# Optimization experiments

Measured on AMD Instinct MI355X. Metric: run time of the kernel, lower is better.

## Reference

```python
import jax, jax.numpy as jnp
import numpy as np

EMB, HID, SEQ = 768, 512, 2048
BATCH = 2
EPS = 1e-6
LN_EPS = 1e-5
ROPE_BASE = 10000.0
NEG_BIG = -1e9  # stands in for -inf diagonal mask (identical entmax output, NaN-safe)


def rotate_half(x):
    d = x.shape[-1] // 2
    return jnp.concatenate([-x[..., d:], x[..., :d]], axis=-1)


def rope_tables(L, D, dtype=jnp.float32):
    inv_freq = 1.0 / (ROPE_BASE ** (jnp.arange(0, D, 2, dtype=jnp.float32) / D))
    t = jnp.arange(L, dtype=jnp.float32)
    freqs = jnp.outer(t, inv_freq)            # [L, D/2]
    emb = jnp.concatenate([freqs, freqs], -1)  # [L, D]
    return jnp.cos(emb).astype(dtype), jnp.sin(emb).astype(dtype)


def layernorm(x, gamma, beta):
    mu = jnp.mean(x, axis=-1, keepdims=True)
    var = jnp.mean(jnp.square(x - mu), axis=-1, keepdims=True)
    return (x - mu) * jax.lax.rsqrt(var + LN_EPS) * gamma + beta


def entmax15(z):
    """Exact 1.5-entmax along last axis (Peters & Martins sort algorithm)."""
    z = z / 2.0
    z = z - jnp.max(z, axis=-1, keepdims=True)
    zs = -jnp.sort(-z, axis=-1)                      # descending
    L = z.shape[-1]
    k = jnp.arange(1, L + 1, dtype=z.dtype)
    cum = jnp.cumsum(zs, axis=-1)
    cum2 = jnp.cumsum(zs * zs, axis=-1)
    mean = cum / k
    ss = cum2 - cum * mean                           # k*(E[x^2]-E[x]^2)
    delta = (1.0 - ss) / k
    tau = mean - jnp.sqrt(jnp.maximum(delta, 0.0))
    support = jnp.sum((tau <= zs).astype(jnp.int32), axis=-1)
    tau_star = jnp.take_along_axis(tau, (support - 1)[..., None], axis=-1)
    return jnp.square(jnp.maximum(z - tau_star, 0.0))


def setup_inputs() -> dict:
    key = jax.random.key(0)
    ks = jax.random.split(key, 3)
    x = jax.random.normal(ks[0], (BATCH, SEQ, EMB), dtype=jnp.float32)
    Wq = jax.random.normal(ks[1], (HID, EMB), dtype=jnp.float32) / np.sqrt(EMB)
    Wk = jax.random.normal(ks[2], (HID, EMB), dtype=jnp.float32) / np.sqrt(EMB)
    return {
        "x": x, "Wq": Wq, "Wk": Wk,
        "q_gamma": jnp.ones((HID,), jnp.float32), "q_beta": jnp.zeros((HID,), jnp.float32),
        "k_gamma": jnp.ones((HID,), jnp.float32), "k_beta": jnp.zeros((HID,), jnp.float32),
        "C_weight": jnp.ones((1,), jnp.float32),
        "F_weight": jnp.ones((1,), jnp.float32),
        "S_weight": jnp.ones((1,), jnp.float32),
    }


def reference(x, Wq, Wk, q_gamma, q_beta, k_gamma, k_beta, C_weight, F_weight, S_weight):
    B, L, _ = x.shape
    q = layernorm(x @ Wq.T, q_gamma, q_beta)   # [B,L,D]
    k = layernorm(x @ Wk.T, k_gamma, k_beta)
    cos, sin = rope_tables(L, q.shape[-1], q.dtype)
    q = q * cos + rotate_half(q) * sin
    k = k * cos + rotate_half(k) * sin

    wC = 2.0 * jax.nn.sigmoid(C_weight)
    wF = 2.0 * jax.nn.sigmoid(F_weight)
    wS = 2.0 * jax.nn.sigmoid(S_weight)

    Gkk = jnp.einsum('bld,ble->bde', k, k)     # [B,D,D]
    Gkq = jnp.einsum('bld,ble->bde', k, q)
    Gqq = jnp.einsum('bld,ble->bde', q, q)

    C_raw = jnp.einsum('bid,bde,bje->bij', q, Gkk, q)  # [B,L,L]
    F_raw = jnp.einsum('bid,bde,bje->bij', q, Gkq, k)
    S_raw = jnp.einsum('bid,bde,bje->bij', k, Gqq, k)

    C = C_raw - jnp.mean(C_raw, axis=-1, keepdims=True)
    Fm = F_raw - jnp.mean(F_raw, axis=-1, keepdims=True)
    S = S_raw - jnp.mean(S_raw, axis=-1, keepdims=True)

    pC = jnp.clip(entmax15(wC * C), 0.0, 1.0 - EPS)
    pF = jnp.clip(entmax15(wF * Fm), 0.0, 1.0 - EPS)
    pS = jnp.clip(entmax15(wS * S), 0.0, 1.0 - EPS)

    pC = pC * jax.lax.rsqrt(jnp.sum(pC, axis=-2, keepdims=True) + EPS)
    pS = pS * jax.lax.rsqrt(jnp.sum(pS, axis=-2, keepdims=True) + EPS)

    pC = jnp.maximum((1.0 - 2.0 * EPS) * pC + EPS, EPS)
    pF = jnp.maximum((1.0 - 2.0 * EPS) * pF + EPS, EPS)
    pS = jnp.maximum((1.0 - 2.0 * EPS) * pS + EPS, EPS)

    H = (jnp.log(pC) + jnp.log(pF) + jnp.log(pS)) / 3.0
    diag = jnp.eye(L, dtype=bool)[None]
    H = jnp.where(diag, NEG_BIG, H)
    H = entmax15(H)
    return H, pC, pF, pS
```

## Files before the change

kernel.cpp:

```cpp
#include <hip/hip_runtime.h>
#include <cstddef>
#include <math.h>

#define B_   2
#define L_   2048
#define D_   512
#define E_   768
static const size_t LL   = (size_t)L_ * L_;
static const size_t SLOT = (size_t)B_ * LL;

#define QK_N  ((size_t)B_ * L_ * D_)
#define G1_N  ((size_t)512 * 512)
#define G_N   ((size_t)6 * G1_N)
#define U_N   ((size_t)6 * L_ * D_)
#define X_N   ((size_t)4096 * 768)
#define W_N   ((size_t)512 * 768)

typedef unsigned short u16;
typedef __attribute__((ext_vector_type(8))) _Float16 half8;
typedef __attribute__((ext_vector_type(4))) float f32x4;

__device__ __forceinline__ void split2(float f, u16& h0, u16& h1) {
    _Float16 a = (_Float16)f;
    _Float16 b = (_Float16)((f - (float)a) * 4096.0f);
    h0 = __builtin_bit_cast(u16, a);
    h1 = __builtin_bit_cast(u16, b);
}

#define BKP 40

__device__ __forceinline__ void pstage_MK(const u16* __restrict__ P, size_t pstride, int ld,
                                          int r0, int k0, int tid, u16 S[2][64][BKP]) {
    int m = tid >> 2, kq = (tid & 3) << 3;
#pragma unroll
    for (int s = 0; s < 2; ++s) {
        const uint4 v = *reinterpret_cast<const uint4*>(
            P + (size_t)s * pstride + (size_t)(r0 + m) * ld + k0 + kq);
        *reinterpret_cast<uint4*>(&S[s][m][kq]) = v;
    }
}
__device__ __forceinline__ void pstage_KM(const u16* __restrict__ P, size_t pstride, int ld,
                                          int r0, int k0, int tid, u16 S[2][64][BKP]) {
    int k = tid >> 3, mq = (tid & 7) << 3;
#pragma unroll
    for (int s = 0; s < 2; ++s) {
        const uint4 v = *reinterpret_cast<const uint4*>(
            P + (size_t)s * pstride + (size_t)(k0 + k) * ld + r0 + mq);
        const u16* pv = reinterpret_cast<const u16*>(&v);
#pragma unroll
        for (int c = 0; c < 8; ++c) S[s][mq + c][k] = pv[c];
    }
}

template<bool AKM, bool BKM, bool PROM>
__device__ __forceinline__ void gemm_core(const u16* __restrict__ Ap, size_t Aps, int lda,
                                          const u16* __restrict__ Bp, size_t Bps, int ldb,
                                          int K, int m0, int n0, int tid,
                                          double outv[2][2][4]) {
    __shared__ u16 SA[2][64][BKP], SB[2][64][BKP];
    f32x4 accH[2][2], accM[2][2];
#pragma unroll
    for (int i = 0; i < 2; ++i)
#pragma unroll
        for (int j = 0; j < 2; ++j) {
            accH[i][j] = (f32x4){0.f, 0.f, 0.f, 0.f};
            accM[i][j] = (f32x4){0.f, 0.f, 0.f, 0.f};
        }
    double accD[2][2][4] = {};
    int lane = tid & 63, w = tid >> 6;
    int wm = (w & 1) << 5, wn = (w >> 1) << 5;
    int fr = lane & 15, ko = (lane >> 4) << 3;

    int nstep = K >> 5;
    for (int s = 0; s < nstep; ++s) {
        int k0 = s << 5;
        if (AKM) pstage_KM(Ap, Aps, lda, m0, k0, tid, SA); else pstage_MK(Ap, Aps, lda, m0, k0, tid, SA);
        if (BKM) pstage_KM(Bp, Bps, ldb, n0, k0, tid, SB); else pstage_MK(Bp, Bps, ldb, n0, k0, tid, SB);
        __syncthreads();
        half8 a[2][2], b[2][2];
#pragma unroll
        for (int f = 0; f < 2; ++f)
#pragma unroll
            for (int sp = 0; sp < 2; ++sp) {
                a[f][sp] = *reinterpret_cast<const half8*>(&SA[sp][wm + f * 16 + fr][ko]);
                b[f][sp] = *reinterpret_cast<const half8*>(&SB[sp][wn + f * 16 + fr][ko]);
            }
#pragma unroll
        for (int fi = 0; fi < 2; ++fi)
#pragma unroll
            for (int fj = 0; fj < 2; ++fj) {
                accH[fi][fj] = __builtin_amdgcn_mfma_f32_16x16x32_f16(a[fi][0], b[fj][0], accH[fi][fj], 0, 0, 0);
                accM[fi][fj] = __builtin_amdgcn_mfma_f32_16x16x32_f16(a[fi][0], b[fj][1], accM[fi][fj], 0, 0, 0);
                accM[fi][fj] = __builtin_amdgcn_mfma_f32_16x16x32_f16(a[fi][1], b[fj][0], accM[fi][fj], 0, 0, 0);
            }
        __syncthreads();
        if (PROM) {
#pragma unroll
            for (int fi = 0; fi < 2; ++fi)
#pragma unroll
                for (int fj = 0; fj < 2; ++fj) {
#pragma unroll
                    for (int r = 0; r < 4; ++r) accD[fi][fj][r] += (double)accH[fi][fj][r];
                    accH[fi][fj] = (f32x4){0.f, 0.f, 0.f, 0.f};
                }
        }
    }
    const double S1 = 1.0 / 4096.0;
#pragma unroll
    for (int fi = 0; fi < 2; ++fi)
#pragma unroll
        for (int fj = 0; fj < 2; ++fj)
#pragma unroll
            for (int r = 0; r < 4; ++r)
                outv[fi][fj][r] = (PROM ? accD[fi][fj][r] : (double)accH[fi][fj][r])
                                + (double)accM[fi][fj][r] * S1;
}

typedef const __attribute__((address_space(1))) void gas_void;
typedef __attribute__((address_space(3))) void las_void;

__device__ __forceinline__ void gload16(const u16* g, u16* l) {
    __builtin_amdgcn_global_load_lds((gas_void*)g, (las_void*)l, 16, 0, 0);
}

__device__ __forceinline__ void gstage128(const u16* __restrict__ P, size_t pstride, int ld,
                                          int r0, int k0, int lane, int w,
                                          u16 S[2][128][32]) {
#pragma unroll
    for (int sp = 0; sp < 2; ++sp)
#pragma unroll
        for (int t = 0; t < 2; ++t) {
            int rb = (w << 5) + (t << 4);
            int row = rb + (lane >> 2);
            int chunk = (lane & 3) ^ ((row >> 1) & 3);
            const u16* src = P + (size_t)sp * pstride + (size_t)(r0 + row) * ld
                             + (k0 + (chunk << 3));
            gload16(src, &S[sp][rb][0]);
        }
}

__device__ __forceinline__ void gemm128(const u16* __restrict__ Ap, size_t Aps, int lda,
                                        const u16* __restrict__ Bp, size_t Bps, int ldb,
                                        int K, int m0, int n0, int tid,
                                        float* __restrict__ out, int ldo) {
    __shared__ u16 SA[2][128][32], SB[2][128][32];
    f32x4 accH[4][4], accM[4][4];
#pragma unroll
    for (int i = 0; i < 4; ++i)
#pragma unroll
        for (int j = 0; j < 4; ++j) {
            accH[i][j] = (f32x4){0.f, 0.f, 0.f, 0.f};
            accM[i][j] = (f32x4){0.f, 0.f, 0.f, 0.f};
        }
    int lane = tid & 63, w = tid >> 6;
    int wm = (w & 1) << 6, wn = (w >> 1) << 6;
    int fr = lane & 15, ko8 = lane >> 4;

    int nstep = K >> 5;
    for (int s = 0; s < nstep; ++s) {
        int k0 = s << 5;
        gstage128(Ap, Aps, lda, m0, k0, lane, w, SA);
        gstage128(Bp, Bps, ldb, n0, k0, lane, w, SB);
        __syncthreads();
        half8 a[4][2], b[4][2];
#pragma unroll
        for (int f = 0; f < 4; ++f) {
            int ra = wm + (f << 4) + fr;
            int rbn = wn + (f << 4) + fr;
            int ca = (ko8 ^ ((ra >> 1) & 3)) << 3;
            int cb = (ko8 ^ ((rbn >> 1) & 3)) << 3;
#pragma unroll
            for (int sp = 0; sp < 2; ++sp) {
                a[f][sp] = *reinterpret_cast<const half8*>(&SA[sp][ra][ca]);
                b[f][sp] = *reinterpret_cast<const half8*>(&SB[sp][rbn][cb]);
            }
        }
#pragma unroll
        for (int fi = 0; fi < 4; ++fi)
#pragma unroll
            for (int fj = 0; fj < 4; ++fj) {
                accH[fi][fj] = __builtin_amdgcn_mfma_f32_16x16x32_f16(a[fi][0], b[fj][0], accH[fi][fj], 0, 0, 0);
                accM[fi][fj] = __builtin_amdgcn_mfma_f32_16x16x32_f16(a[fi][0], b[fj][1], accM[fi][fj], 0, 0, 0);
                accM[fi][fj] = __builtin_amdgcn_mfma_f32_16x16x32_f16(a[fi][1], b[fj][0], accM[fi][fj], 0, 0, 0);
            }
        __syncthreads();
    }
    const double S1 = 1.0 / 4096.0;
    int col = lane & 15, rbase = (lane >> 4) << 2;
#pragma unroll
    for (int fi = 0; fi < 4; ++fi)
#pragma unroll
        for (int fj = 0; fj < 4; ++fj)
#pragma unroll
            for (int r = 0; r < 4; ++r) {
                int mm = m0 + wm + (fi << 4) + rbase + r;
                int nn = n0 + wn + (fj << 4) + col;
                out[(size_t)mm * ldo + nn] =
                    (float)((double)accH[fi][fj][r] + (double)accM[fi][fj][r] * S1);
            }
}

__global__ __launch_bounds__(256) void k_prep(const float* __restrict__ x,
                                              const float* __restrict__ Wq,
                                              const float* __restrict__ Wk,
                                              u16* __restrict__ xP,
                                              u16* __restrict__ WP,
                                              double* __restrict__ tg) {
    int bx = blockIdx.x;
    if (bx < L_) {
        int l = bx, j = threadIdx.x;
        double e = (double)j * (1.0 / 256.0);
        double inv = pow(10000.0, -e);
        double ang = (double)l * inv;
        tg[(size_t)l * 512 + j] = cos(ang);
        tg[(size_t)l * 512 + 256 + j] = sin(ang);
        return;
    }
    size_t gid = (size_t)(bx - L_) * 256 + threadIdx.x;
    const size_t XH = X_N / 2, WH = W_N / 2;
    const float* src; u16* dst; size_t pn, off;
    if (gid < XH)            { src = x  + 2 * gid;              dst = xP;            pn = X_N; off = 2 * gid; }
    else if (gid < XH + WH)  { size_t g = gid - XH;      src = Wq + 2 * g; dst = WP;            pn = W_N; off = 2 * g; }
    else                     { size_t g = gid - XH - WH; src = Wk + 2 * g; dst = WP + 2 * W_N;  pn = W_N; off = 2 * g; }
    float2 v = *reinterpret_cast<const float2*>(src);
    u16 a0, a1, b0, b1;
    split2(v.x, a0, a1);
    split2(v.y, b0, b1);
    *reinterpret_cast<unsigned*>(dst + off)      = (unsigned)a0 | ((unsigned)b0 << 16);
    *reinterpret_cast<unsigned*>(dst + pn + off) = (unsigned)a1 | ((unsigned)b1 << 16);
}

__global__ __launch_bounds__(256, 2) void k_proj(const u16* __restrict__ xP,
                                                 const u16* __restrict__ WP,
                                                 float* __restrict__ qraw,
                                                 float* __restrict__ kraw) {
    int z = blockIdx.z;
    float* out = z ? kraw : qraw;
    const u16* Bp = WP + (size_t)z * 2 * W_N;
    gemm128(xP, X_N, E_, Bp, W_N, E_, E_,
            blockIdx.y * 128, blockIdx.x * 128, threadIdx.x, out, D_);
}

__global__ __launch_bounds__(256) void k_lnrope(const float* __restrict__ qraw,
                                                const float* __restrict__ kraw,
                                                const double* __restrict__ tg,
                                                const float* __restrict__ qg, const float* __restrict__ qb,
                                                const float* __restrict__ kg, const float* __restrict__ kb,
                                                u16* __restrict__ qP, u16* __restrict__ kP) {
    int row = blockIdx.x;
    int l = row & (L_ - 1);
    int tid = threadIdx.x;
    int half = tid >> 7, t = tid & 127;
    __shared__ double nrow[2][D_];
    __shared__ double red[8];
    __shared__ double cs_[256], sn_[256];
    {
        int j = tid & 255;
        if (tid < 256) { cs_[j] = tg[(size_t)l * 512 + j]; sn_[j] = tg[(size_t)l * 512 + 256 + j]; }
    }
    const float* rp = (half ? kraw : qraw) + (size_t)row * D_;
    const float* g  = half ? kg : qg;
    const float* bt = half ? kb : qb;
    u16* P = half ? kP : qP;
    float4 v = reinterpret_cast<const float4*>(rp)[t];
    double vv[4] = {(double)v.x, (double)v.y, (double)v.z, (double)v.w};
    double s = vv[0] + vv[1] + vv[2] + vv[3];
    double s2 = vv[0]*vv[0] + vv[1]*vv[1] + vv[2]*vv[2] + vv[3]*vv[3];
    for (int off = 32; off; off >>= 1) { s += __shfl_xor(s, off); s2 += __shfl_xor(s2, off); }
    int wv = tid >> 6;
    if ((tid & 63) == 0) { red[wv * 2] = s; red[wv * 2 + 1] = s2; }
    __syncthreads();
    double mu  = (red[half * 4 + 0] + red[half * 4 + 2]) * (1.0 / D_);
    double var = (red[half * 4 + 1] + red[half * 4 + 3]) * (1.0 / D_) - mu * mu;
    double rs = rsqrt(var + 1e-5);
    int d0 = t * 4;
    double o[4];
#pragma unroll
    for (int c = 0; c < 4; ++c) {
        int d = d0 + c;
        o[c] = (vv[c] - mu) * rs * (double)g[d] + (double)bt[d];
    }
#pragma unroll
    for (int c = 0; c < 4; ++c) nrow[half][d0 + c] = o[c];
    __syncthreads();
    u16 h[2][4];
#pragma unroll
    for (int c = 0; c < 4; ++c) {
        int d = d0 + c;
        double rot = (d < 256) ? -nrow[half][d + 256] : nrow[half][d - 256];
        float ov = (float)(nrow[half][d] * cs_[d & 255] + rot * sn_[d & 255]);
        split2(ov, h[0][c], h[1][c]);
    }
    size_t off = (size_t)row * D_ + d0;
#pragma unroll
    for (int sp = 0; sp < 2; ++sp)
        *reinterpret_cast<ushort4*>(P + sp * QK_N + off) = make_ushort4(h[sp][0], h[sp][1], h[sp][2], h[sp][3]);
}

__global__ __launch_bounds__(256) void k_gram(const u16* __restrict__ qP,
                                              const u16* __restrict__ kP,
                                              float* __restrict__ Gpart) {
    int zz = blockIdx.z, half = zz & 1, z = zz >> 1;
    int b = z / 3, m = z % 3;
    const u16* A  = ((m == 2) ? qP : kP) + (size_t)b * L_ * D_ + (size_t)half * (L_ / 2) * D_;
    const u16* Bp = ((m == 0) ? kP : qP) + (size_t)b * L_ * D_ + (size_t)half * (L_ / 2) * D_;
    int m0 = blockIdx.y * 64, n0 = blockIdx.x * 64;
    double ov[2][2][4];
    gemm_core<true, true, true>(A, QK_N, D_, Bp, QK_N, D_, L_ / 2, m0, n0, threadIdx.x, ov);
    float* Gg = Gpart + (size_t)half * G_N + (size_t)z * G1_N;
    int lane = threadIdx.x & 63, w = threadIdx.x >> 6;
    int wm = (w & 1) << 5, wn = (w >> 1) << 5;
    int col = lane & 15, rbase = (lane >> 4) << 2;
#pragma unroll
    for (int fi = 0; fi < 2; ++fi)
#pragma unroll
        for (int fj = 0; fj < 2; ++fj)
#pragma unroll
            for (int r = 0; r < 4; ++r) {
                int mm = m0 + wm + fi * 16 + rbase + r;
                int nn = n0 + wn + fj * 16 + col;
                Gg[(size_t)mm * 512 + nn] = (float)ov[fi][fj][r];
            }
}

__global__ __launch_bounds__(256) void k_gsplitT(const float* __restrict__ Gpart,
                                                 u16* __restrict__ GPT) {
    __shared__ float T[64][65];
    int z = blockIdx.z, d0 = blockIdx.y * 64, e0 = blockIdx.x * 64;
    const float* Ga = Gpart + (size_t)z * G1_N;
    const float* Gb = Ga + G_N;
    int tid = threadIdx.x;
#pragma unroll
    for (int i = 0; i < 16; ++i) {
        int idx = tid + i * 256;
        int r = idx >> 6, c = idx & 63;
        size_t o = (size_t)(d0 + r) * 512 + e0 + c;
        T[r][c] = Ga[o] + Gb[o];
    }
    __syncthreads();
    u16* Gz = GPT + (size_t)z * G1_N;
#pragma unroll
    for (int i = 0; i < 16; ++i) {
        int idx = tid + i * 256;
        int er = idx >> 6, dc = idx & 63;
        u16 h0, h1; split2(T[dc][er], h0, h1);
        size_t o = (size_t)(e0 + er) * 512 + d0 + dc;
        Gz[o] = h0; Gz[G_N + o] = h1;
    }
}

__global__ __launch_bounds__(256) void k_u(const u16* __restrict__ qP,
                                           const u16* __restrict__ kP,
                                           const u16* __restrict__ GPT,
                                           u16* __restrict__ UP) {
    int z = blockIdx.z, b = z / 3, m = z % 3;
    const u16* A  = ((m == 2) ? kP : qP) + (size_t)b * L_ * D_;
    const u16* Bp = GPT + (size_t)z * G1_N;
    int m0 = blockIdx.y * 64, n0 = blockIdx.x * 64;
    double ov[2][2][4];
    gemm_core<false, false, true>(A, QK_N, D_, Bp, G_N, 512, D_, m0, n0, threadIdx.x, ov);
    int lane = threadIdx.x & 63, w = threadIdx.x >> 6;
    int wm = (w & 1) << 5, wn = (w >> 1) << 5;
    int col = lane & 15, rbase = (lane >> 4) << 2;
#pragma unroll
    for (int fi = 0; fi < 2; ++fi)
#pragma unroll
        for (int fj = 0; fj < 2; ++fj)
#pragma unroll
            for (int r = 0; r < 4; ++r) {
                float uf = (float)ov[fi][fj][r];
                int mm = m0 + wm + fi * 16 + rbase + r;
                int nn = n0 + wn + fj * 16 + col;
                size_t off = (size_t)z * ((size_t)L_ * D_) + (size_t)mm * D_ + nn;
                u16 h0, h1; split2(uf, h0, h1);
                UP[off] = h0; UP[U_N + off] = h1;
            }
}

__global__ __launch_bounds__(256, 2) void k_scores(const u16* __restrict__ qP,
                                                   const u16* __restrict__ kP,
                                                   const u16* __restrict__ UP,
                                                   float* __restrict__ out) {
    int z = blockIdx.z, b = z / 3, m = z % 3;
    const u16* A  = UP + (size_t)z * ((size_t)L_ * D_);
    const u16* Bp = ((m == 0) ? qP : kP) + (size_t)b * L_ * D_;
    float* Co = out + (size_t)(1 + m) * SLOT + (size_t)b * LL;
    gemm128(A, U_N, D_, Bp, QK_N, D_, D_,
            blockIdx.y * 128, blockIdx.x * 128, threadIdx.x, Co, L_);
}

__global__ __launch_bounds__(256) void k_entmax(float* __restrict__ base, int nrows,
                                                const float* __restrict__ wC,
                                                const float* __restrict__ wF,
                                                const float* __restrict__ wS) {
    int tid = threadIdx.x;
    int lane = tid & 63;
    int r = blockIdx.x * 4 + (tid >> 6);
    if (r >= nrows) return;
    int m = r >> 12;
    const float* wp = (m == 0) ? wC : (m == 1) ? wF : wS;
    float hw = (float)(1.0 / (1.0 + exp(-(double)wp[0])));
    float* row = base + (size_t)r * L_;
    float v[32];
    float mx = -3.4e38f;
#pragma unroll
    for (int j = 0; j < 32; ++j) {
        v[j] = row[lane + (j << 6)];
        mx = fmaxf(mx, v[j]);
    }
    for (int off = 32; off; off >>= 1) mx = fmaxf(mx, __shfl_xor(mx, off));
    float z[32];
#pragma unroll
    for (int j = 0; j < 32; ++j) z[j] = hw * (v[j] - mx);
    float lo = -1.0f, hi = 0.0f;
    for (int it = 0; it < 9; ++it) {
        float tau = 0.5f * (lo + hi);
        float ssum = 0.0f;
#pragma unroll
        for (int j = 0; j < 32; ++j) {
            float t = fmaxf(z[j] - tau, 0.0f);
            ssum = fmaf(t, t, ssum);
        }
        for (int off = 32; off; off >>= 1) ssum += __shfl_xor(ssum, off);
        if (ssum >= 1.0f) lo = tau; else hi = tau;
    }
    float tau = lo;
    for (int it = 0; it < 3; ++it) {
        float s1 = 0.0f, s2 = 0.0f;
#pragma unroll
        for (int j = 0; j < 32; ++j) {
            float t = fmaxf(z[j] - tau, 0.0f);
            s1 += t;
            s2 = fmaf(t, t, s2);
        }
        for (int off = 32; off; off >>= 1) { s1 += __shfl_xor(s1, off); s2 += __shfl_xor(s2, off); }
        float denom = 2.0f * s1;
        if (denom > 1e-30f) tau += fmaxf((s2 - 1.0f) / denom, 0.0f);
    }
#pragma unroll
    for (int j = 0; j < 32; ++j) {
        float t = fmaxf(z[j] - tau, 0.0f);
        row[lane + (j << 6)] = fminf(t * t, 1.0f - 1e-6f);
    }
}

__global__ __launch_bounds__(256) void k_colsum(const float* __restrict__ out,
                                                double* __restrict__ part) {
    int bz = blockIdx.z, which = bz >> 1, b = bz & 1;
    const float* mat = out + (size_t)(which ? 3 : 1) * SLOT + (size_t)b * LL;
    int j = blockIdx.x * 256 + threadIdx.x;
    int r0 = blockIdx.y * 128;
    double s = 0.0;
#pragma unroll 8
    for (int r = 0; r < 128; ++r) s += (double)mat[(size_t)(r0 + r) * L_ + j];
    part[((size_t)bz * 16 + blockIdx.y) * L_ + j] = s;
}

__global__ __launch_bounds__(256) void k_colred(const double* __restrict__ part,
                                                double* __restrict__ csC,
                                                double* __restrict__ csS) {
    int g = blockIdx.x * 256 + threadIdx.x;
    int bz = g >> 11, j = g & (L_ - 1);
    int which = bz >> 1, b = bz & 1;
    double s = 0.0;
#pragma unroll
    for (int c = 0; c < 16; ++c) s += part[((size_t)bz * 16 + c) * L_ + j];
    (which ? csS : csC)[b * L_ + j] = s;
}

__global__ __launch_bounds__(256) void k_fin2(float* __restrict__ out,
                                              const double* __restrict__ csC,
                                              const double* __restrict__ csS) {
    int row = blockIdx.x;
    int i = row & (L_ - 1), b = row >> 11;
    size_t ro = (size_t)row * L_;
    float* H  = out + ro;
    float* pC = out + SLOT + ro;
    float* pF = out + 2 * SLOT + ro;
    float* pS = out + 3 * SLOT + ro;
    const double* cc = csC + b * L_;
    const double* cs = csS + b * L_;
    int tid = threadIdx.x, lane = tid & 63, wv = tid >> 6;
    __shared__ float red[4], red2[4];
    const double A1 = 1.0 - 2e-6;
    float h[8];
    float mx = -3.4e38f;
#pragma unroll
    for (int c = 0; c < 8; ++c) {
        int j = (c << 8) + tid;
        double cv = (double)pC[j] * rsqrt(cc[j] + 1e-6);
        double fv = (double)pF[j];
        double sv = (double)pS[j] * rsqrt(cs[j] + 1e-6);
        cv = fmax(A1 * cv + 1e-6, 1e-6);
        fv = fmax(A1 * fv + 1e-6, 1e-6);
        sv = fmax(A1 * sv + 1e-6, 1e-6);
        pC[j] = (float)cv; pF[j] = (float)fv; pS[j] = (float)sv;
        h[c] = (j == i) ? -1e9f : logf((float)(cv * fv * sv)) * (1.0f / 3.0f);
        mx = fmaxf(mx, h[c]);
    }
    for (int off = 32; off; off >>= 1) mx = fmaxf(mx, __shfl_xor(mx, off));
    if (lane == 0) red[wv] = mx;
    __syncthreads();
    mx = fmaxf(fmaxf(red[0], red[1]), fmaxf(red[2], red[3]));
    __syncthreads();
    float z[8];
#pragma unroll
    for (int c = 0; c < 8; ++c) z[c] = 0.5f * (h[c] - mx);
    float lo = -1.0f, hi = 0.0f;
    for (int it = 0; it < 9; ++it) {
        float tau = 0.5f * (lo + hi);
        float ssum = 0.0f;
#pragma unroll
        for (int c = 0; c < 8; ++c) {
            float t = fmaxf(z[c] - tau, 0.0f);
            ssum = fmaf(t, t, ssum);
        }
        for (int off = 32; off; off >>= 1) ssum += __shfl_xor(ssum, off);
        if (lane == 0) red[wv] = ssum;
        __syncthreads();
        ssum = red[0] + red[1] + red[2] + red[3];
        __syncthreads();
        if (ssum >= 1.0f) lo = tau; else hi = tau;
    }
    float tau = lo;
    for (int it = 0; it < 3; ++it) {
        float s1 = 0.0f, s2 = 0.0f;
#pragma unroll
        for (int c = 0; c < 8; ++c) {
            float t = fmaxf(z[c] - tau, 0.0f);
            s1 += t;
            s2 = fmaf(t, t, s2);
        }
        for (int off = 32; off; off >>= 1) { s1 += __shfl_xor(s1, off); s2 += __shfl_xor(s2, off); }
        if (lane == 0) { red[wv] = s1; red2[wv] = s2; }
        __syncthreads();
        s1 = red[0] + red[1] + red[2] + red[3];
        s2 = red2[0] + red2[1] + red2[2] + red2[3];
        __syncthreads();
        float denom = 2.0f * s1;
        if (denom > 1e-30f) tau += fmaxf((s2 - 1.0f) / denom, 0.0f);
    }
#pragma unroll
    for (int c = 0; c < 8; ++c) {
        float t = fmaxf(z[c] - tau, 0.0f);
        H[(c << 8) + tid] = t * t;
    }
}

extern "C" void kernel_launch(void* const* d_in, const int* in_sizes, int n_in,
                              void* d_out, int out_size, void* d_ws, size_t ws_size,
                              hipStream_t stream) {
    const float* x  = (const float*)d_in[0];
    const float* Wq = (const float*)d_in[1];
    const float* Wk = (const float*)d_in[2];
    const float* qg = (const float*)d_in[3];
    const float* qb = (const float*)d_in[4];
    const float* kg = (const float*)d_in[5];
    const float* kb = (const float*)d_in[6];
    const float* wC = (const float*)d_in[7];
    const float* wF = (const float*)d_in[8];
    const float* wS = (const float*)d_in[9];
    float* out = (float*)d_out;

    char* wsb = (char*)d_ws;
    u16*    UP   = (u16*)wsb;
    float*  qraw = (float*)wsb;
    float*  kraw = qraw + QK_N;
    float*  Gpart = (float*)(wsb + 2 * QK_N * sizeof(float));
    wsb += 3 * U_N * sizeof(u16);
    u16*    qP    = (u16*)wsb;
    u16*    xP    = (u16*)wsb;   wsb += 3 * QK_N * sizeof(u16);
    u16*    kP    = (u16*)wsb;   wsb += 3 * QK_N * sizeof(u16);
    u16*    GPT   = (u16*)wsb;
    u16*    WP    = (u16*)wsb;   wsb += 3 * G_N * sizeof(u16);
    double* tg    = (double*)wsb;
    double* part  = tg;
    double* csC   = tg + (size_t)4 * 16 * L_;
    double* csS   = csC + (size_t)B_ * L_;

    k_prep    <<<dim3(L_ + 7680), 256, 0, stream>>>(x, Wq, Wk, xP, WP, tg);
    k_proj    <<<dim3(4, 32, 2),  256, 0, stream>>>(xP, WP, qraw, kraw);
    k_lnrope  <<<dim3(B_ * L_),   256, 0, stream>>>(qraw, kraw, tg, qg, qb, kg, kb, qP, kP);
    k_gram    <<<dim3(8, 8, 12),  256, 0, stream>>>(qP, kP, Gpart);
    k_gsplitT <<<dim3(8, 8, 6),   256, 0, stream>>>(Gpart, GPT);
    k_u       <<<dim3(8, 32, 6),  256, 0, stream>>>(qP, kP, GPT, UP);
    k_scores  <<<dim3(16, 16, 6), 256, 0, stream>>>(qP, kP, UP, out);
    k_entmax  <<<dim3(3072),      256, 0, stream>>>(out + SLOT, 3 * B_ * L_, wC, wF, wS);
    k_colsum  <<<dim3(8, 16, 4),  256, 0, stream>>>(out, part);
    k_colred  <<<dim3(32),        256, 0, stream>>>(part, csC, csS);
    k_fin2    <<<dim3(B_ * L_),   256, 0, stream>>>(out, csC, csS);
}
```

Baseline: 546.6 us.

## Pre-transpose q/k and stage GEMM tiles with direct global-to-LDS loads

Adds a transpose kernel that writes D-major copies of the split-half q and k into scratch space the projection stage no longer needs, so the Gram GEMM can read K-contiguous rows. The old register-staged LDS loader, including its scalar transposing path, is replaced by a shared GEMM routine. That routine uses global_load_lds 16-byte loads into an XOR-swizzled, unpadded LDS layout, and both the Gram and U kernels now use it. This removes the strided element-wise LDS transposes and the register round-trip on staging. The cost is an extra kernel launch plus a full read and write of q and k.

```diff
diff --git a/kernel.cpp b/kernel.cpp
--- a/kernel.cpp
+++ b/kernel.cpp
@@ -27,37 +27,19 @@
     h1 = __builtin_bit_cast(u16, b);
 }
 
-#define BKP 40
-
-__device__ __forceinline__ void pstage_MK(const u16* __restrict__ P, size_t pstride, int ld,
-                                          int r0, int k0, int tid, u16 S[2][64][BKP]) {
-    int m = tid >> 2, kq = (tid & 3) << 3;
-#pragma unroll
-    for (int s = 0; s < 2; ++s) {
-        const uint4 v = *reinterpret_cast<const uint4*>(
-            P + (size_t)s * pstride + (size_t)(r0 + m) * ld + k0 + kq);
-        *reinterpret_cast<uint4*>(&S[s][m][kq]) = v;
-    }
-}
-__device__ __forceinline__ void pstage_KM(const u16* __restrict__ P, size_t pstride, int ld,
-                                          int r0, int k0, int tid, u16 S[2][64][BKP]) {
-    int k = tid >> 3, mq = (tid & 7) << 3;
-#pragma unroll
-    for (int s = 0; s < 2; ++s) {
-        const uint4 v = *reinterpret_cast<const uint4*>(
-            P + (size_t)s * pstride + (size_t)(k0 + k) * ld + r0 + mq);
-        const u16* pv = reinterpret_cast<const u16*>(&v);
-#pragma unroll
-        for (int c = 0; c < 8; ++c) S[s][mq + c][k] = pv[c];
-    }
-}
-
-template<bool AKM, bool BKM, bool PROM>
-__device__ __forceinline__ void gemm_core(const u16* __restrict__ Ap, size_t Aps, int lda,
-                                          const u16* __restrict__ Bp, size_t Bps, int ldb,
-                                          int K, int m0, int n0, int tid,
-                                          double outv[2][2][4]) {
-    __shared__ u16 SA[2][64][BKP], SB[2][64][BKP];
+typedef const __attribute__((address_space(1))) void gas_void;
+typedef __attribute__((address_space(3))) void las_void;
+
+__device__ __forceinline__ void gload16(const u16* g, u16* l) {
+    __builtin_amdgcn_global_load_lds((gas_void*)g, (las_void*)l, 16, 0, 0);
+}
+
+template<bool PROM>
+__device__ __forceinline__ void gemm64g(const u16* __restrict__ Ap, size_t Aps, int lda,
+                                        const u16* __restrict__ Bp, size_t Bps, int ldb,
+                                        int K, int m0, int n0, int tid,
+                                        double outv[2][2][4]) {
+    __shared__ u16 SA[2][64][32], SB[2][64][32];
     f32x4 accH[2][2], accM[2][2];
 #pragma unroll
     for (int i = 0; i < 2; ++i)
@@ -69,22 +51,36 @@
     double accD[2][2][4] = {};
     int lane = tid & 63, w = tid >> 6;
     int wm = (w & 1) << 5, wn = (w >> 1) << 5;
-    int fr = lane & 15, ko = (lane >> 4) << 3;
+    int fr = lane & 15, ko8 = lane >> 4;
+
+    int rb = w << 4;
+    int srow = rb + (lane >> 2);
+    int schunk = (lane & 3) ^ ((srow >> 1) & 3);
 
     int nstep = K >> 5;
     for (int s = 0; s < nstep; ++s) {
         int k0 = s << 5;
-        if (AKM) pstage_KM(Ap, Aps, lda, m0, k0, tid, SA); else pstage_MK(Ap, Aps, lda, m0, k0, tid, SA);
-        if (BKM) pstage_KM(Bp, Bps, ldb, n0, k0, tid, SB); else pstage_MK(Bp, Bps, ldb, n0, k0, tid, SB);
+#pragma unroll
+        for (int sp = 0; sp < 2; ++sp) {
+            gload16(Ap + (size_t)sp * Aps + (size_t)(m0 + srow) * lda + k0 + (schunk << 3),
+                    &SA[sp][rb][0]);
+            gload16(Bp + (size_t)sp * Bps + (size_t)(n0 + srow) * ldb + k0 + (schunk << 3),
+                    &SB[sp][rb][0]);
+        }
         __syncthreads();
         half8 a[2][2], b[2][2];
 #pragma unroll
-        for (int f = 0; f < 2; ++f)
+        for (int f = 0; f < 2; ++f) {
+            int ra = wm + f * 16 + fr;
+            int rbn = wn + f * 16 + fr;
+            int ca = (ko8 ^ ((ra >> 1) & 3)) << 3;
+            int cb = (ko8 ^ ((rbn >> 1) & 3)) << 3;
 #pragma unroll
             for (int sp = 0; sp < 2; ++sp) {
-                a[f][sp] = *reinterpret_cast<const half8*>(&SA[sp][wm + f * 16 + fr][ko]);
-                b[f][sp] = *reinterpret_cast<const half8*>(&SB[sp][wn + f * 16 + fr][ko]);
+                a[f][sp] = *reinterpret_cast<const half8*>(&SA[sp][ra][ca]);
+                b[f][sp] = *reinterpret_cast<const half8*>(&SB[sp][rbn][cb]);
             }
+        }
 #pragma unroll
         for (int fi = 0; fi < 2; ++fi)
 #pragma unroll
@@ -114,13 +110,6 @@
             for (int r = 0; r < 4; ++r)
                 outv[fi][fj][r] = (PROM ? accD[fi][fj][r] : (double)accH[fi][fj][r])
                                 + (double)accM[fi][fj][r] * S1;
-}
-
-typedef const __attribute__((address_space(1))) void gas_void;
-typedef __attribute__((address_space(3))) void las_void;
-
-__device__ __forceinline__ void gload16(const u16* g, u16* l) {
-    __builtin_amdgcn_global_load_lds((gas_void*)g, (las_void*)l, 16, 0, 0);
 }
 
 __device__ __forceinline__ void gstage128(const u16* __restrict__ P, size_t pstride, int ld,
@@ -297,16 +286,47 @@
         *reinterpret_cast<ushort4*>(P + sp * QK_N + off) = make_ushort4(h[sp][0], h[sp][1], h[sp][2], h[sp][3]);
 }
 
-__global__ __launch_bounds__(256) void k_gram(const u16* __restrict__ qP,
-                                              const u16* __restrict__ kP,
+__global__ __launch_bounds__(256) void k_qkT(const u16* __restrict__ qP,
+                                             const u16* __restrict__ kP,
+                                             u16* __restrict__ qPT,
+                                             u16* __restrict__ kPT) {
+    __shared__ u16 T[64][72];
+    int z = blockIdx.z;
+    int b = z & 1, sp = (z >> 1) & 1, tn = z >> 2;
+    const u16* src = (tn ? kP : qP) + (size_t)sp * QK_N + (size_t)b * L_ * D_;
+    u16* dst       = (tn ? kPT : qPT) + (size_t)sp * QK_N + (size_t)b * D_ * L_;
+    int l0 = blockIdx.x * 64, d0 = blockIdx.y * 64;
+    int tid = threadIdx.x;
+#pragma unroll
+    for (int i = 0; i < 2; ++i) {
+        int idx = tid + i * 256;
+        int lr = idx >> 3, dc8 = (idx & 7) << 3;
+        *reinterpret_cast<uint4*>(&T[lr][dc8]) =
+            *reinterpret_cast<const uint4*>(&src[(size_t)(l0 + lr) * D_ + d0 + dc8]);
+    }
+    __syncthreads();
+#pragma unroll
+    for (int i = 0; i < 2; ++i) {
+        int idx = tid + i * 256;
+        int dr = idx >> 3, lc8 = (idx & 7) << 3;
+        u16 tmp[8];
+#pragma unroll
+        for (int c = 0; c < 8; ++c) tmp[c] = T[lc8 + c][dr];
+        *reinterpret_cast<uint4*>(&dst[(size_t)(d0 + dr) * L_ + l0 + lc8]) =
+            *reinterpret_cast<const uint4*>(tmp);
+    }
+}
+
+__global__ __launch_bounds__(256) void k_gram(const u16* __restrict__ qPT,
+                                              const u16* __restrict__ kPT,
                                               float* __restrict__ Gpart) {
     int zz = blockIdx.z, half = zz & 1, z = zz >> 1;
     int b = z / 3, m = z % 3;
-    const u16* A  = ((m == 2) ? qP : kP) + (size_t)b * L_ * D_ + (size_t)half * (L_ / 2) * D_;
-    const u16* Bp = ((m == 0) ? kP : qP) + (size_t)b * L_ * D_ + (size_t)half * (L_ / 2) * D_;
+    const u16* A  = ((m == 2) ? qPT : kPT) + (size_t)b * D_ * L_ + (size_t)half * (L_ / 2);
+    const u16* Bp = ((m == 0) ? kPT : qPT) + (size_t)b * D_ * L_ + (size_t)half * (L_ / 2);
     int m0 = blockIdx.y * 64, n0 = blockIdx.x * 64;
     double ov[2][2][4];
-    gemm_core<true, true, true>(A, QK_N, D_, Bp, QK_N, D_, L_ / 2, m0, n0, threadIdx.x, ov);
+    gemm64g<true>(A, QK_N, L_, Bp, QK_N, L_, L_ / 2, m0, n0, threadIdx.x, ov);
     float* Gg = Gpart + (size_t)half * G_N + (size_t)z * G1_N;
     int lane = threadIdx.x & 63, w = threadIdx.x >> 6;
     int wm = (w & 1) << 5, wn = (w >> 1) << 5;
@@ -358,7 +378,7 @@
     const u16* Bp = GPT + (size_t)z * G1_N;
     int m0 = blockIdx.y * 64, n0 = blockIdx.x * 64;
     double ov[2][2][4];
-    gemm_core<false, false, true>(A, QK_N, D_, Bp, G_N, 512, D_, m0, n0, threadIdx.x, ov);
+    gemm64g<true>(A, QK_N, D_, Bp, G_N, 512, D_, m0, n0, threadIdx.x, ov);
     int lane = threadIdx.x & 63, w = threadIdx.x >> 6;
     int wm = (w & 1) << 5, wn = (w >> 1) << 5;
     int col = lane & 15, rbase = (lane >> 4) << 2;
@@ -566,6 +586,8 @@
     u16*    UP   = (u16*)wsb;
     float*  qraw = (float*)wsb;
     float*  kraw = qraw + QK_N;
+    u16*    qPT  = (u16*)wsb;
+    u16*    kPT  = qPT + 2 * QK_N;
     float*  Gpart = (float*)(wsb + 2 * QK_N * sizeof(float));
     wsb += 3 * U_N * sizeof(u16);
     u16*    qP    = (u16*)wsb;
@@ -581,7 +603,8 @@
     k_prep    <<<dim3(L_ + 7680), 256, 0, stream>>>(x, Wq, Wk, xP, WP, tg);
     k_proj    <<<dim3(4, 32, 2),  256, 0, stream>>>(xP, WP, qraw, kraw);
     k_lnrope  <<<dim3(B_ * L_),   256, 0, stream>>>(qraw, kraw, tg, qg, qb, kg, kb, qP, kP);
-    k_gram    <<<dim3(8, 8, 12),  256, 0, stream>>>(qP, kP, Gpart);
+    k_qkT     <<<dim3(32, 8, 8),  256, 0, stream>>>(qP, kP, qPT, kPT);
+    k_gram    <<<dim3(8, 8, 12),  256, 0, stream>>>(qPT, kPT, Gpart);
     k_gsplitT <<<dim3(8, 8, 6),   256, 0, stream>>>(Gpart, GPT);
     k_u       <<<dim3(8, 32, 6),  256, 0, stream>>>(qP, kP, GPT, UP);
     k_scores  <<<dim3(16, 16, 6), 256, 0, stream>>>(qP, kP, UP, out);
```

After: 476.6 us. 12.8% less time.
